# Optimization experiments

Hardware: AMD Instinct MI355X
Metric: run time of the kernel (lower is better)

## Reference

```python
import math
import jax, jax.numpy as jnp
import numpy as np
from jax import lax

W_DIM = 512
UP = 2
K = 3
LRELU_GAIN = math.sqrt(2.0)  # bias_act def_gain for 'lrelu'
CLAMP = 256.0                # conv_clamp * gain(=1)


def setup_inputs() -> dict:
    key = jax.random.key(0)
    ks = jax.random.split(key, 8)
    B, Cin, Cout, H = 16, 512, 512, 32
    return {
        "x": jax.random.normal(ks[0], (B, Cin, H, H), jnp.float32),
        "w_latent": jax.random.normal(ks[1], (B, W_DIM), jnp.float32),
        "affine_weight": jax.random.normal(ks[2], (Cin, W_DIM), jnp.float32),
        "affine_bias": jnp.ones((Cin,), jnp.float32),  # bias_init=1
        "conv_weight": jax.random.normal(ks[3], (Cout, Cin, K, K), jnp.float32),
        "noise": jax.random.normal(ks[4], (B, 1, 2 * H, 2 * H), jnp.float32),
        "noise_strength": jax.random.uniform(ks[5], (1,), jnp.float32),
        "bias": jax.random.normal(ks[6], (Cout,), jnp.float32),
    }


def reference(x, w_latent, affine_weight, affine_bias, conv_weight, noise, noise_strength, bias):
    B, Cin, H, W = x.shape
    Cout = conv_weight.shape[0]

    # EqualFullyConnectedLayer (linear act): style = w @ (W * 1/sqrt(in)).T + b
    style = w_latent @ (affine_weight * (1.0 / math.sqrt(W_DIM))).T + affine_bias  # [B, Cin]

    # Modulate + demodulate per-sample weights: [B, Cout, Cin, K, K]
    wmod = conv_weight[None] * style[:, None, :, None, None]
    dcoefs = lax.rsqrt(jnp.sum(wmod * wmod, axis=(2, 3, 4)) + 1e-8)  # [B, Cout]
    wmod = wmod * dcoefs[:, :, None, None, None]

    # Grouped transposed conv (stride=UP), batch-as-groups trick.
    # torch.conv_transpose2d(x, w.transpose, stride=UP) == dilated conv with
    # spatially-flipped modulated weight, lhs_dilation=UP, padding=K-1.
    w_eff = wmod.reshape(B * Cout, Cin, K, K)[:, :, ::-1, ::-1]
    x1 = x.reshape(1, B * Cin, H, W)
    y = lax.conv_general_dilated(
        x1, w_eff, window_strides=(1, 1),
        padding=[(K - 1, K - 1), (K - 1, K - 1)],
        lhs_dilation=(UP, UP), feature_group_count=B,
        dimension_numbers=("NCHW", "OIHW", "NCHW"))  # [1, B*Cout, 2H+1, 2W+1]

    # upfirdn2d: FIR low-pass (1,3,3,1) outer, normalized, gain=up^2, pad (1,1,1,1)
    f1 = jnp.array([1.0, 3.0, 3.0, 1.0], jnp.float32)
    f2 = jnp.outer(f1, f1)
    f2 = f2 / f2.sum() * (UP * UP)
    yc = y.reshape(B * Cout, 1, 2 * H + 1, 2 * W + 1)
    y = lax.conv_general_dilated(
        yc, f2[None, None], window_strides=(1, 1), padding=[(1, 1), (1, 1)],
        dimension_numbers=("NCHW", "OIHW", "NCHW"))
    y = y.reshape(B, Cout, 2 * H, 2 * W)

    # noise injection + fused bias + lrelu(gain=sqrt(2)) + clamp
    y = y + noise * noise_strength[0]
    y = y + bias[None, :, None, None]
    y = jax.nn.leaky_relu(y, negative_slope=0.2) * LRELU_GAIN
    return jnp.clip(y, -CLAMP, CLAMP)
```

## Files before the change

kernel.cpp:

```cpp
#include <hip/hip_runtime.h>
#include <hip/hip_bf16.h>


typedef unsigned short u16;
typedef unsigned int u32;
typedef u16 u16x8 __attribute__((ext_vector_type(8)));
typedef __bf16 bf16x8 __attribute__((ext_vector_type(8)));
typedef float f32x4 __attribute__((ext_vector_type(4)));

#define NB 16

__device__ __forceinline__ float bf2f(u16 v) {
  unsigned int u = ((unsigned int)v) << 16;
  float f;
  __builtin_memcpy(&f, &u, 4);
  return f;
}
__device__ __forceinline__ u16 f2bf(float f) {
  __hip_bfloat16 h = __float2bfloat16(f);
  u16 r;
  __builtin_memcpy(&r, &h, 2);
  return r;
}
__device__ __forceinline__ void async16(u16* lds, const u16* g) {
  __builtin_amdgcn_global_load_lds(
      (const __attribute__((address_space(1))) u32*)g,
      (__attribute__((address_space(3))) u32*)lds, 16, 0, 0);
}

__global__ __launch_bounds__(256) void k_style(const float* __restrict__ wl,
                                               const float* __restrict__ aw,
                                               const float* __restrict__ ab,
                                               float* __restrict__ style) {
  __shared__ float lw[512];
  const int b = blockIdx.y;
  const int c = blockIdx.x * 256 + threadIdx.x;
  for (int k = threadIdx.x; k < 512; k += 256) lw[k] = wl[b * 512 + k];
  __syncthreads();
  const float* row = aw + (size_t)c * 512;
  float acc = 0.f;
#pragma unroll 8
  for (int k = 0; k < 512; ++k) acc += lw[k] * row[k];
  style[b * 512 + c] = acc * 0.04419417382415922f + ab[c];
}

__global__ __launch_bounds__(256) void k_dcoef(const float* __restrict__ cw,
                                               const float* __restrict__ style,
                                               float* __restrict__ dcoef) {
  __shared__ float wsq[512];
  const int o = blockIdx.x, t = threadIdx.x;
  for (int c = t; c < 512; c += 256) {
    const float* p = cw + (size_t)o * 4608 + (size_t)c * 9;
    float s = 0.f;
#pragma unroll
    for (int k = 0; k < 9; ++k) {
      float v = p[k];
      s += v * v;
    }
    wsq[c] = s;
  }
  __syncthreads();
  const int w = t >> 6, l = t & 63;
  for (int b = w; b < NB; b += 4) {
    float part = 0.f;
#pragma unroll
    for (int c = l; c < 512; c += 64) {
      float st = style[b * 512 + c];
      part += st * st * wsq[c];
    }
#pragma unroll
    for (int off = 32; off; off >>= 1) part += __shfl_down(part, off, 64);
    if (l == 0) dcoef[b * 512 + o] = 1.0f / sqrtf(part + 1e-8f);
  }
}

__global__ __launch_bounds__(256) void k_pack(const float* __restrict__ cw,
                                              u16* __restrict__ W2) {
  __shared__ u16 lw[4608];
  const int o = blockIdx.x, t = threadIdx.x;
  const float* src = cw + (size_t)o * 4608;
  for (int v = t; v < 4608; v += 256) {
    unsigned c = (unsigned)v / 9u;
    unsigned kp = (unsigned)v % 9u;
    lw[kp * 512 + c] = f2bf(src[v]);
  }
  __syncthreads();
  u16* dst = W2 + (size_t)o * 4608;
  for (int v = t; v < 576; v += 256)
    *(u16x8*)(dst + v * 8) = *(const u16x8*)(lw + v * 8);
}

__global__ __launch_bounds__(256) void k_xt(const float* __restrict__ x,
                                            const float* __restrict__ style,
                                            u16* __restrict__ xT) {
  __shared__ u16 tile[64 * 66];
  const int b = blockIdx.z, c0 = blockIdx.y << 6, s0 = blockIdx.x << 6;
  const int t = threadIdx.x;
#pragma unroll
  for (int i = 0; i < 16; ++i) {
    int e = i * 256 + t;
    int cc = e >> 6, ss = e & 63;
    int c = c0 + cc;
    float v = x[(size_t)(b * 512 + c) * 1024 + s0 + ss] * style[b * 512 + c];
    tile[cc * 66 + ss] = f2bf(v);
  }
  __syncthreads();
#pragma unroll
  for (int i = 0; i < 16; ++i) {
    int e = i * 256 + t;
    int sc = e >> 6, cx = e & 63;
    xT[(size_t)(b * 1024 + s0 + sc) * 512 + c0 + cx] = tile[cx * 66 + sc];
  }
}

__global__ __launch_bounds__(256) void k_gemm(const u16* __restrict__ W2,
                                              const u16* __restrict__ xT,
                                              u16* __restrict__ Z) {
  __shared__ u16 At[128 * 32];
  __shared__ u16 Bt[128 * 32];
  const int t = threadIdx.x;
  const int m0 = blockIdx.y << 7;
  const int n0 = blockIdx.x << 7;
  const int l = t & 63;
  const int w = t >> 6;
  const int wy = ((t >> 7) & 1) << 6;
  const int wx = ((t >> 6) & 1) << 6;
  const int lrow = l & 15;
  const int lk8 = (l >> 4) << 3;

  const u16* gA = W2 + (size_t)(m0 + (t >> 2)) * 512 + ((t & 3) << 3);
  const u16* gB = xT + (size_t)(n0 + (t >> 2)) * 512 + ((t & 3) << 3);
  u16* lA0 = At + (w << 9);
  u16* lA1 = At + 2048 + (w << 9);
  u16* lB0 = Bt + (w << 9);
  u16* lB1 = Bt + 2048 + (w << 9);

  f32x4 acc[4][4] = {};

  for (int k0 = 0; k0 < 512; k0 += 32) {
    async16(lA0, gA + k0);
    async16(lA1, gA + k0 + 64 * 512);
    async16(lB0, gB + k0);
    async16(lB1, gB + k0 + 64 * 512);
    asm volatile("s_waitcnt vmcnt(0)" ::: "memory");
    __syncthreads();
    bf16x8 av[4], bv[4];
#pragma unroll
    for (int i = 0; i < 4; ++i)
      av[i] = *(const bf16x8*)(At + (wy + i * 16 + lrow) * 32 + lk8);
#pragma unroll
    for (int j = 0; j < 4; ++j)
      bv[j] = *(const bf16x8*)(Bt + (wx + j * 16 + lrow) * 32 + lk8);
#pragma unroll
    for (int i = 0; i < 4; ++i)
#pragma unroll
      for (int j = 0; j < 4; ++j)
        acc[i][j] = __builtin_amdgcn_mfma_f32_16x16x32_bf16(av[i], bv[j], acc[i][j], 0, 0, 0);
    __syncthreads();
  }

  const int mr = m0 + wy + ((l >> 4) << 2);
  const int nc = n0 + wx + lrow;
#pragma unroll
  for (int i = 0; i < 4; ++i)
#pragma unroll
    for (int j = 0; j < 4; ++j)
#pragma unroll
      for (int r = 0; r < 4; ++r)
        Z[(size_t)(mr + i * 16 + r) * 16384 + nc + j * 16] = f2bf(acc[i][j][r]);
}

__global__ __launch_bounds__(256) void k_scatter(
    const u16* __restrict__ Z, const float* __restrict__ dcoef,
    const float* __restrict__ noise, const float* __restrict__ nstr,
    const float* __restrict__ bias, float* __restrict__ out) {
  __shared__ u16 Zl[9 * 1024];
  __shared__ float Hl[3 * 2048];
  const int o = blockIdx.x;
  const int b = blockIdx.y;
  const int t = threadIdx.x;
  const u16* Zp = Z + (size_t)o * 9 * 16384 + (size_t)b * 1024;
  for (int v = t; v < 1152; v += 256) {
    int kp = v >> 7, off = (v & 127) << 3;
    *(u16x8*)(Zl + kp * 1024 + off) = *(const u16x8*)(Zp + (size_t)kp * 16384 + off);
  }
  __syncthreads();
#pragma unroll
  for (int e = 0; e < 12; ++e) {
    int idx = e * 256 + t;
    int ky = idx >> 10;
    int i = (idx >> 5) & 31;
    int j = idx & 31;
    const u16* P0 = Zl + (ky * 3 + 0) * 1024 + i * 32;
    const u16* P1 = P0 + 1024;
    const u16* P2 = P0 + 2048;
    float Ej = bf2f(P0[j]) + (j >= 1 ? bf2f(P2[j - 1]) : 0.f);
    float Ej1 = (j < 31 ? bf2f(P0[j + 1]) : 0.f) + bf2f(P2[j]);
    float Ojm = j >= 1 ? bf2f(P1[j - 1]) : 0.f;
    float Oj = bf2f(P1[j]);
    float Ojp = j < 31 ? bf2f(P1[j + 1]) : 0.f;
    float* hp = Hl + ky * 2048 + i * 64 + j;
    hp[0] = Ojm + 3.f * Ej + 3.f * Oj + Ej1;
    hp[32] = Ej + 3.f * Oj + 3.f * Ej1 + Ojp;
  }
  __syncthreads();
  const float dc = dcoef[b * 512 + o] * 0.0625f;
  const float ns = nstr[0];
  const float bo = bias[o];
  const int n = t & 63;
  const int i0 = (t >> 6) << 3;
  const int sw = ((n & 1) << 5) | (n >> 1);
  const float* H0 = Hl + sw;
  const float* H1 = Hl + 2048 + sw;
  const float* H2 = Hl + 4096 + sw;
  float h0 = H0[i0 * 64];
  float h1 = H1[i0 * 64];
  float h1p = (i0 > 0) ? H1[(i0 - 1) * 64] : 0.f;
  float h2p = (i0 > 0) ? H2[(i0 - 1) * 64] : 0.f;
  const float* nz = noise + ((size_t)b << 12) + n;
  float* op = out + (((size_t)(b * 512 + o)) << 12) + n;
#pragma unroll
  for (int s = 0; s < 8; ++s) {
    int i = i0 + s;
    float h0n = (i < 31) ? H0[(i + 1) * 64] : 0.f;
    float h1n = (i < 31) ? H1[(i + 1) * 64] : 0.f;
    float h2 = H2[i * 64];
    float ev = h1p + 3.f * (h0 + h2p) + 3.f * h1 + (h0n + h2);
    float od = (h0 + h2p) + 3.f * h1 + 3.f * (h0n + h2) + h1n;
    int m = 2 * i;
    float v0 = ev * dc + nz[(size_t)m * 64] * ns + bo;
    v0 = (v0 > 0.f ? v0 : 0.2f * v0) * 1.4142135623730951f;
    v0 = fminf(fmaxf(v0, -256.f), 256.f);
    op[(size_t)m * 64] = v0;
    float v1 = od * dc + nz[(size_t)(m + 1) * 64] * ns + bo;
    v1 = (v1 > 0.f ? v1 : 0.2f * v1) * 1.4142135623730951f;
    v1 = fminf(fmaxf(v1, -256.f), 256.f);
    op[(size_t)(m + 1) * 64] = v1;
    h0 = h0n;
    h1p = h1;
    h1 = h1n;
    h2p = h2;
  }
}

extern "C" void kernel_launch(void* const* d_in, const int* in_sizes, int n_in,
                              void* d_out, int out_size, void* d_ws, size_t ws_size,
                              hipStream_t stream) {
  const float* x = (const float*)d_in[0];
  const float* wl = (const float*)d_in[1];
  const float* aw = (const float*)d_in[2];
  const float* ab = (const float*)d_in[3];
  const float* cw = (const float*)d_in[4];
  const float* noise = (const float*)d_in[5];
  const float* nstr = (const float*)d_in[6];
  const float* bias = (const float*)d_in[7];
  float* out = (float*)d_out;

  float* style = (float*)d_ws;
  float* dcoef = style + 8192;
  u16* W2 = (u16*)(dcoef + 8192);
  u16* xT = W2 + 4608 * 512;
  u16* Z = xT + (size_t)16384 * 512;

  k_style<<<dim3(2, 16), 256, 0, stream>>>(wl, aw, ab, style);
  k_dcoef<<<dim3(512), 256, 0, stream>>>(cw, style, dcoef);
  k_pack<<<dim3(512), 256, 0, stream>>>(cw, W2);
  k_xt<<<dim3(16, 8, 16), 256, 0, stream>>>(x, style, xT);
  k_gemm<<<dim3(128, 36), 256, 0, stream>>>(W2, xT, Z);
  k_scatter<<<dim3(512, 16), 256, 0, stream>>>(Z, dcoef, noise, nstr, bias, out);
}
```

Baseline: 383.6 us.

## Fuse weight prep kernels, vectorize transpose stores, swizzle GEMM LDS layout

Merges the demodulation-coefficient and weight-packing kernels into one launch that reads the conv weights once. Changes the transpose kernel to write 16-byte vectors instead of scalar u16 stores. Applies an XOR-like rotation swizzle to the GEMM's LDS tile chunks, on both the async load side and the MFMA fragment read side, to reduce bank conflicts. The swizzle has to be consistent on both sides or results are wrong.

```diff
diff --git a/kernel.cpp b/kernel.cpp
--- a/kernel.cpp
+++ b/kernel.cpp
@@ -44,39 +44,12 @@
   style[b * 512 + c] = acc * 0.04419417382415922f + ab[c];
 }
 
-__global__ __launch_bounds__(256) void k_dcoef(const float* __restrict__ cw,
+__global__ __launch_bounds__(256) void k_wprep(const float* __restrict__ cw,
                                                const float* __restrict__ style,
-                                               float* __restrict__ dcoef) {
+                                               float* __restrict__ dcoef,
+                                               u16* __restrict__ W2) {
+  __shared__ u16 lw[4608];
   __shared__ float wsq[512];
-  const int o = blockIdx.x, t = threadIdx.x;
-  for (int c = t; c < 512; c += 256) {
-    const float* p = cw + (size_t)o * 4608 + (size_t)c * 9;
-    float s = 0.f;
-#pragma unroll
-    for (int k = 0; k < 9; ++k) {
-      float v = p[k];
-      s += v * v;
-    }
-    wsq[c] = s;
-  }
-  __syncthreads();
-  const int w = t >> 6, l = t & 63;
-  for (int b = w; b < NB; b += 4) {
-    float part = 0.f;
-#pragma unroll
-    for (int c = l; c < 512; c += 64) {
-      float st = style[b * 512 + c];
-      part += st * st * wsq[c];
-    }
-#pragma unroll
-    for (int off = 32; off; off >>= 1) part += __shfl_down(part, off, 64);
-    if (l == 0) dcoef[b * 512 + o] = 1.0f / sqrtf(part + 1e-8f);
-  }
-}
-
-__global__ __launch_bounds__(256) void k_pack(const float* __restrict__ cw,
-                                              u16* __restrict__ W2) {
-  __shared__ u16 lw[4608];
   const int o = blockIdx.x, t = threadIdx.x;
   const float* src = cw + (size_t)o * 4608;
   for (int v = t; v < 4608; v += 256) {
@@ -84,10 +57,32 @@
     unsigned kp = (unsigned)v % 9u;
     lw[kp * 512 + c] = f2bf(src[v]);
   }
+  for (int c = t; c < 512; c += 256) {
+    const float* p = src + (size_t)c * 9;
+    float s = 0.f;
+#pragma unroll
+    for (int k = 0; k < 9; ++k) {
+      float v = p[k];
+      s += v * v;
+    }
+    wsq[c] = s;
+  }
   __syncthreads();
   u16* dst = W2 + (size_t)o * 4608;
   for (int v = t; v < 576; v += 256)
     *(u16x8*)(dst + v * 8) = *(const u16x8*)(lw + v * 8);
+  const int w = t >> 6, l = t & 63;
+  for (int b = w; b < NB; b += 4) {
+    float part = 0.f;
+#pragma unroll
+    for (int c = l; c < 512; c += 64) {
+      float st = style[b * 512 + c];
+      part += st * st * wsq[c];
+    }
+#pragma unroll
+    for (int off = 32; off; off >>= 1) part += __shfl_down(part, off, 64);
+    if (l == 0) dcoef[b * 512 + o] = 1.0f / sqrtf(part + 1e-8f);
+  }
 }
 
 __global__ __launch_bounds__(256) void k_xt(const float* __restrict__ x,
@@ -106,10 +101,14 @@
   }
   __syncthreads();
 #pragma unroll
-  for (int i = 0; i < 16; ++i) {
-    int e = i * 256 + t;
-    int sc = e >> 6, cx = e & 63;
-    xT[(size_t)(b * 1024 + s0 + sc) * 512 + c0 + cx] = tile[cx * 66 + sc];
+  for (int e = 0; e < 2; ++e) {
+    int idx = e * 256 + t;
+    int sc = idx >> 3;
+    int cg = (idx & 7) << 3;
+    u16x8 v;
+#pragma unroll
+    for (int g = 0; g < 8; ++g) v[g] = tile[(cg + g) * 66 + sc];
+    *(u16x8*)(xT + (size_t)(b * 1024 + s0 + sc) * 512 + c0 + cg) = v;
   }
 }
 
@@ -126,14 +125,17 @@
   const int wy = ((t >> 7) & 1) << 6;
   const int wx = ((t >> 6) & 1) << 6;
   const int lrow = l & 15;
-  const int lk8 = (l >> 4) << 3;
-
-  const u16* gA = W2 + (size_t)(m0 + (t >> 2)) * 512 + ((t & 3) << 3);
-  const u16* gB = xT + (size_t)(n0 + (t >> 2)) * 512 + ((t & 3) << 3);
+
+  const int sr = t >> 2;
+  const int sch = ((t & 3) + (sr >> 1)) & 3;
+  const u16* gA = W2 + (size_t)(m0 + sr) * 512 + (sch << 3);
+  const u16* gB = xT + (size_t)(n0 + sr) * 512 + (sch << 3);
   u16* lA0 = At + (w << 9);
   u16* lA1 = At + 2048 + (w << 9);
   u16* lB0 = Bt + (w << 9);
   u16* lB1 = Bt + 2048 + (w << 9);
+
+  const int sk8 = (((l >> 4) - (lrow >> 1)) & 3) << 3;
 
   f32x4 acc[4][4] = {};
 
@@ -147,10 +149,10 @@
     bf16x8 av[4], bv[4];
 #pragma unroll
     for (int i = 0; i < 4; ++i)
-      av[i] = *(const bf16x8*)(At + (wy + i * 16 + lrow) * 32 + lk8);
+      av[i] = *(const bf16x8*)(At + (wy + i * 16 + lrow) * 32 + sk8);
 #pragma unroll
     for (int j = 0; j < 4; ++j)
-      bv[j] = *(const bf16x8*)(Bt + (wx + j * 16 + lrow) * 32 + lk8);
+      bv[j] = *(const bf16x8*)(Bt + (wx + j * 16 + lrow) * 32 + sk8);
 #pragma unroll
     for (int i = 0; i < 4; ++i)
 #pragma unroll
@@ -263,8 +265,7 @@
   u16* Z = xT + (size_t)16384 * 512;
 
   k_style<<<dim3(2, 16), 256, 0, stream>>>(wl, aw, ab, style);
-  k_dcoef<<<dim3(512), 256, 0, stream>>>(cw, style, dcoef);
-  k_pack<<<dim3(512), 256, 0, stream>>>(cw, W2);
+  k_wprep<<<dim3(512), 256, 0, stream>>>(cw, style, dcoef, W2);
   k_xt<<<dim3(16, 8, 16), 256, 0, stream>>>(x, style, xT);
   k_gemm<<<dim3(128, 36), 256, 0, stream>>>(W2, xT, Z);
   k_scatter<<<dim3(512, 16), 256, 0, stream>>>(Z, dcoef, noise, nstr, bias, out);
```

Result: no change. 379.6 us (-1.0%).
